# Kernel tuning notes

Measured on AMD Instinct MI355X. Metric: run time of the kernel, lower is better.

The kernel has to match this reference:

```python
import jax, jax.numpy as jnp
import numpy as np

N = 4194304          # flat pixel batch (~2 full 1080p frames)
NUM_CAMERAS = 8
NUM_FRAMES = 1000
EPS = 1e-6


def setup_inputs() -> dict:
    key = jax.random.key(0)
    ks = jax.random.split(key, 8)
    W, H = 1920, 1080
    exposure_params = 0.2 * jax.random.normal(ks[0], (NUM_FRAMES,), jnp.float32)
    vignetting_params = 0.05 * jax.random.normal(ks[1], (NUM_CAMERAS, 3, 5), jnp.float32)
    color_params = 0.05 * jax.random.normal(ks[2], (NUM_FRAMES, 8), jnp.float32)
    # CRF raw init matching the module: softplus-inverse of 1.0 with minima (0.3,0.3,0.1), offset 0
    def _sp_inv(x, m):
        return float(np.log(np.expm1(max(1e-5, x - m))))
    crf0 = jnp.array([_sp_inv(1.0, 0.3), _sp_inv(1.0, 0.3), _sp_inv(1.0, 0.1), 0.0], jnp.float32)
    crf_params = (jnp.broadcast_to(crf0, (NUM_CAMERAS, 3, 4))
                  + 0.05 * jax.random.normal(ks[3], (NUM_CAMERAS, 3, 4), jnp.float32))
    rgb = jax.random.uniform(ks[4], (N, 3), jnp.float32)
    pixel_coords = jax.random.uniform(ks[5], (N, 2), jnp.float32) * jnp.array([W, H], jnp.float32)
    camera_idcs = jax.random.randint(ks[6], (N,), 0, NUM_CAMERAS, jnp.int32)
    frame_idcs = jax.random.randint(ks[7], (N,), 0, NUM_FRAMES, jnp.int32)
    return dict(exposure_params=exposure_params, vignetting_params=vignetting_params,
                color_params=color_params, crf_params=crf_params, rgb=rgb,
                pixel_coords=pixel_coords, camera_idcs=camera_idcs, frame_idcs=frame_idcs,
                resolution_w=W, resolution_h=H)


def _ppisp(exposure_params, vignetting_params, color_params, crf_params,
           rgb, pixel_coords, camera_idcs, frame_idcs, resolution_w, resolution_h):
    # 1) per-frame exposure (EV scale)
    exp_scale = jnp.exp2(exposure_params[frame_idcs])[:, None]            # [N,1]
    x = rgb * exp_scale                                                    # [N,3]

    # 2) per-camera, per-channel radial vignetting: params = [cx, cy, a1, a2, a3]
    vig = vignetting_params[camera_idcs]                                   # [N,3,5]
    u = pixel_coords[:, 0] / jnp.float32(resolution_w) - 0.5               # [N]
    v = pixel_coords[:, 1] / jnp.float32(resolution_h) - 0.5               # [N]
    du = u[:, None] - vig[..., 0]                                          # [N,3]
    dv = v[:, None] - vig[..., 1]
    r2 = du * du + dv * dv                                                 # [N,3]
    falloff = 1.0 + r2 * (vig[..., 2] + r2 * (vig[..., 3] + r2 * vig[..., 4]))
    x = x * falloff

    # 3) per-frame color: WB gains (r,b) + off-diagonal 3x3 mixing matrix (8 params)
    cp = color_params[frame_idcs]                                          # [N,8]
    gains = jnp.stack([jnp.exp(cp[:, 0]), jnp.ones_like(cp[:, 0]), jnp.exp(cp[:, 1])], axis=-1)
    x = x * gains
    one = jnp.ones_like(cp[:, 0])
    M = jnp.stack([
        jnp.stack([one,      cp[:, 2], cp[:, 3]], axis=-1),
        jnp.stack([cp[:, 4], one,      cp[:, 5]], axis=-1),
        jnp.stack([cp[:, 6], cp[:, 7], one     ], axis=-1)], axis=-2)      # [N,3,3]
    x = jnp.einsum('nij,nj->ni', M, x)

    # 4) per-camera, per-channel 4-param sigmoid CRF, identity at init
    crf = crf_params[camera_idcs]                                          # [N,3,4]
    a = jax.nn.softplus(crf[..., 0]) + 0.3
    b = jax.nn.softplus(crf[..., 1]) + 0.3
    c = jax.nn.softplus(crf[..., 2]) + 0.1
    d = crf[..., 3]
    xc = jnp.clip(x, EPS, 1.0)
    xa = xc ** a
    out = xa / (xa + (c * (1.0 - xc) + EPS) ** b) + d                      # [N,3]
    return out


def reference(exposure_params, vignetting_params, color_params, crf_params,
              rgb, pixel_coords, camera_idcs, frame_idcs, resolution_w, resolution_h):
    return _ppisp(exposure_params, vignetting_params, color_params, crf_params,
                  rgb, pixel_coords, camera_idcs, frame_idcs, resolution_w, resolution_h)
```

## Files before the change

kernel.cpp:

```cpp
#include <hip/hip_runtime.h>


__device__ __forceinline__ unsigned bf16r(float x) {
    unsigned b = __float_as_uint(x);
    return (b + 0x7fffu + ((b >> 16) & 1u)) >> 16;
}
__device__ __forceinline__ unsigned packbf(float lo, float hi) {
    return bf16r(lo) | (bf16r(hi) << 16);
}
__device__ __forceinline__ float ulo(unsigned u) { return __uint_as_float(u << 16); }
__device__ __forceinline__ float uhi(unsigned u) { return __uint_as_float(u & 0xffff0000u); }

__global__ void ppisp_precompute(const float* __restrict__ expo,
                                 const float* __restrict__ colorp,
                                 const float* __restrict__ vigp,
                                 const float* __restrict__ crfp,
                                 unsigned* __restrict__ ftab,
                                 float* __restrict__ camtab,
                                 int num_frames, int ncam) {
    int tid = blockIdx.x * blockDim.x + threadIdx.x;
    if (tid < num_frames) {
        float e = exp2f(expo[tid]);
        const float* cp = colorp + tid * 8;
        float g_r = e * expf(cp[0]);
        float g_b = e * expf(cp[1]);
        unsigned* f = ftab + tid * 6;
        f[0] = packbf(g_r, e);
        f[1] = packbf(g_b, cp[2]);
        f[2] = packbf(cp[3], cp[4]);
        f[3] = packbf(cp[5], cp[6]);
        f[4] = packbf(cp[7], 0.f);
        f[5] = 0u;
    }
    if (tid < ncam * 3) {
        int c = tid / 3, ch = tid % 3;
        const float* vp = vigp + tid * 5;
        const float* cf = crfp + tid * 4;
        float* r = camtab + c * 28 + ch * 9;
        r[0] = vp[0];
        r[1] = vp[1];
        r[2] = vp[2];
        r[3] = vp[3];
        r[4] = vp[4];
        r[5] = log1pf(expf(cf[0])) + 0.3f;
        r[6] = log1pf(expf(cf[1])) + 0.3f;
        r[7] = log1pf(expf(cf[2])) + 0.1f;
        r[8] = cf[3];
        if (ch == 0) camtab[c * 28 + 27] = 0.f;
    }
}

__global__ __launch_bounds__(256, 5) void ppisp_main(
    const float4* __restrict__ rgb4,
    const float4* __restrict__ pc4,
    const int4*   __restrict__ cam4,
    const int4*   __restrict__ frm4,
    const uint2*  __restrict__ ftab2,
    const float4* __restrict__ camtab4,
    const int*    __restrict__ resw,
    const int*    __restrict__ resh,
    float4* __restrict__ out4,
    int ngroups, int groups_per_block, int num_frames, int ncam) {
    __shared__ uint2  sft[3000];
    __shared__ float4 scam[56];

    int tid = threadIdx.x;
    int nfw = num_frames * 3;
    for (int i = tid; i < nfw; i += 256) sft[i] = ftab2[i];
    if (tid < ncam * 7) scam[tid] = camtab4[tid];
    __syncthreads();

    float invW = 1.0f / (float)resw[0];
    float invH = 1.0f / (float)resh[0];

    int gbase = blockIdx.x * groups_per_block;
    int gend = gbase + groups_per_block;
    if (gend > ngroups) gend = ngroups;

    for (int g = gbase + tid; g < gend; g += 256) {
        float4 r0  = rgb4[(size_t)g * 3 + 0];
        float4 r1  = rgb4[(size_t)g * 3 + 1];
        float4 r2v = rgb4[(size_t)g * 3 + 2];
        float4 p0  = pc4[(size_t)g * 2 + 0];
        float4 p1  = pc4[(size_t)g * 2 + 1];
        int4 cams = cam4[g];
        int4 frms = frm4[g];

        float rgbp[4][3] = {{r0.x, r0.y, r0.z},
                            {r0.w, r1.x, r1.y},
                            {r1.z, r1.w, r2v.x},
                            {r2v.y, r2v.z, r2v.w}};
        float px[4] = {p0.x, p0.z, p1.x, p1.z};
        float py[4] = {p0.y, p0.w, p1.y, p1.z};
        py[2] = p1.y; py[3] = p1.w;
        py[0] = p0.y; py[1] = p0.w;
        int camA[4] = {cams.x, cams.y, cams.z, cams.w};
        int frmA[4] = {frms.x, frms.y, frms.z, frms.w};

        float o[12];

#pragma unroll
        for (int p = 0; p < 4; ++p) {
            int fb = frmA[p] * 3;
            uint2 A = sft[fb + 0];
            uint2 B = sft[fb + 1];
            unsigned Cw = sft[fb + 2].x;
            float g_r = ulo(A.x), g_g = uhi(A.x), g_b = ulo(A.y);
            float m01 = uhi(A.y), m02 = ulo(B.x), m10 = uhi(B.x);
            float m12 = ulo(B.y), m20 = uhi(B.y), m21 = ulo(Cw);

            int cb = camA[p] * 7;
            float4 q0 = scam[cb + 0];
            float4 q1 = scam[cb + 1];
            float4 q2 = scam[cb + 2];
            float4 q3 = scam[cb + 3];
            float4 q4 = scam[cb + 4];
            float4 q5 = scam[cb + 5];
            float4 q6 = scam[cb + 6];

            float u = px[p] * invW - 0.5f;
            float v = py[p] * invH - 0.5f;

            float cx0 = q0.x, cy0 = q0.y, a10 = q0.z, a20 = q0.w, a30 = q1.x;
            float aa0 = q1.y, bb0 = q1.z, cc0 = q1.w, dd0 = q2.x;
            float cx1 = q2.y, cy1 = q2.z, a11 = q2.w, a21 = q3.x, a31 = q3.y;
            float aa1 = q3.z, bb1 = q3.w, cc1 = q4.x, dd1 = q4.y;
            float cx2 = q4.z, cy2 = q4.w, a12 = q5.x, a22 = q5.y, a32 = q5.z;
            float aa2 = q5.w, bb2 = q6.x, cc2 = q6.y, dd2 = q6.z;

            float du0 = u - cx0, dv0 = v - cy0;
            float du1 = u - cx1, dv1 = v - cy1;
            float du2 = u - cx2, dv2 = v - cy2;
            float r20 = du0 * du0 + dv0 * dv0;
            float r21 = du1 * du1 + dv1 * dv1;
            float r22 = du2 * du2 + dv2 * dv2;
            float fa0 = 1.0f + r20 * (a10 + r20 * (a20 + r20 * a30));
            float fa1 = 1.0f + r21 * (a11 + r21 * (a21 + r21 * a31));
            float fa2 = 1.0f + r22 * (a12 + r22 * (a22 + r22 * a32));

            float x0 = rgbp[p][0] * g_r * fa0;
            float x1 = rgbp[p][1] * g_g * fa1;
            float x2 = rgbp[p][2] * g_b * fa2;

            float y0 = x0 + m01 * x1 + m02 * x2;
            float y1 = m10 * x0 + x1 + m12 * x2;
            float y2 = m20 * x0 + m21 * x1 + x2;

            float xc0 = fminf(fmaxf(y0, 1e-6f), 1.0f);
            float xc1 = fminf(fmaxf(y1, 1e-6f), 1.0f);
            float xc2 = fminf(fmaxf(y2, 1e-6f), 1.0f);

            float xa0 = __builtin_amdgcn_exp2f(aa0 * __builtin_amdgcn_logf(xc0));
            float xa1 = __builtin_amdgcn_exp2f(aa1 * __builtin_amdgcn_logf(xc1));
            float xa2 = __builtin_amdgcn_exp2f(aa2 * __builtin_amdgcn_logf(xc2));
            float t0 = cc0 * (1.0f - xc0) + 1e-6f;
            float t1 = cc1 * (1.0f - xc1) + 1e-6f;
            float t2 = cc2 * (1.0f - xc2) + 1e-6f;
            float tb0 = __builtin_amdgcn_exp2f(bb0 * __builtin_amdgcn_logf(t0));
            float tb1 = __builtin_amdgcn_exp2f(bb1 * __builtin_amdgcn_logf(t1));
            float tb2 = __builtin_amdgcn_exp2f(bb2 * __builtin_amdgcn_logf(t2));

            o[p * 3 + 0] = xa0 * __builtin_amdgcn_rcpf(xa0 + tb0) + dd0;
            o[p * 3 + 1] = xa1 * __builtin_amdgcn_rcpf(xa1 + tb1) + dd1;
            o[p * 3 + 2] = xa2 * __builtin_amdgcn_rcpf(xa2 + tb2) + dd2;
        }

        out4[(size_t)g * 3 + 0] = make_float4(o[0], o[1], o[2], o[3]);
        out4[(size_t)g * 3 + 1] = make_float4(o[4], o[5], o[6], o[7]);
        out4[(size_t)g * 3 + 2] = make_float4(o[8], o[9], o[10], o[11]);
    }
}

extern "C" void kernel_launch(void* const* d_in, const int* in_sizes, int n_in,
                              void* d_out, int out_size, void* d_ws, size_t ws_size,
                              hipStream_t stream) {
    const float* expo   = (const float*)d_in[0];
    const float* vigp   = (const float*)d_in[1];
    const float* colorp = (const float*)d_in[2];
    const float* crfp   = (const float*)d_in[3];
    const float* rgb    = (const float*)d_in[4];
    const float* pc     = (const float*)d_in[5];
    const int*   cam    = (const int*)d_in[6];
    const int*   frm    = (const int*)d_in[7];
    const int*   rw     = (const int*)d_in[8];
    const int*   rh     = (const int*)d_in[9];

    int num_frames = in_sizes[0];
    int ncam = in_sizes[1] / 15;
    int N = in_sizes[4] / 3;

    unsigned* ftab = (unsigned*)d_ws;
    size_t ftab_bytes = ((size_t)num_frames * 6 * sizeof(unsigned) + 255) & ~(size_t)255;
    float* camtab = (float*)((char*)d_ws + ftab_bytes);

    int pre_threads = 256;
    int pre_blocks = (num_frames + pre_threads - 1) / pre_threads;
    if (pre_blocks < 1) pre_blocks = 1;
    ppisp_precompute<<<pre_blocks, pre_threads, 0, stream>>>(
        expo, colorp, vigp, crfp, ftab, camtab, num_frames, ncam);

    int ngroups = N / 4;
    int blocks = 1536;
    int groups_per_block = (ngroups + blocks - 1) / blocks;
    ppisp_main<<<blocks, 256, 0, stream>>>(
        (const float4*)rgb, (const float4*)pc, (const int4*)cam, (const int4*)frm,
        (const uint2*)ftab, (const float4*)camtab, rw, rh, (float4*)d_out,
        ngroups, groups_per_block, num_frames, ncam);
}
```

Before: 182.6 us.

## Fuse table precompute into main kernel and use 1024-thread blocks

Removes the separate precompute launch. Each block now builds the per-frame bf16 table and the per-camera table directly in shared memory, so nothing round-trips through a global workspace. The frame table is repacked into one uint4 plus one float per frame, so each lookup is two LDS reads instead of three. Blocks grow to 1024 threads and the grid shrinks to 512 blocks, which spreads the redundant per-block precompute (exp per frame) over more pixels but cuts scheduling granularity.

```diff
diff --git a/kernel.cpp b/kernel.cpp
--- a/kernel.cpp
+++ b/kernel.cpp
@@ -11,32 +11,44 @@
 __device__ __forceinline__ float ulo(unsigned u) { return __uint_as_float(u << 16); }
 __device__ __forceinline__ float uhi(unsigned u) { return __uint_as_float(u & 0xffff0000u); }
 
-__global__ void ppisp_precompute(const float* __restrict__ expo,
-                                 const float* __restrict__ colorp,
-                                 const float* __restrict__ vigp,
-                                 const float* __restrict__ crfp,
-                                 unsigned* __restrict__ ftab,
-                                 float* __restrict__ camtab,
-                                 int num_frames, int ncam) {
-    int tid = blockIdx.x * blockDim.x + threadIdx.x;
-    if (tid < num_frames) {
-        float e = exp2f(expo[tid]);
-        const float* cp = colorp + tid * 8;
-        float g_r = e * expf(cp[0]);
-        float g_b = e * expf(cp[1]);
-        unsigned* f = ftab + tid * 6;
-        f[0] = packbf(g_r, e);
-        f[1] = packbf(g_b, cp[2]);
-        f[2] = packbf(cp[3], cp[4]);
-        f[3] = packbf(cp[5], cp[6]);
-        f[4] = packbf(cp[7], 0.f);
-        f[5] = 0u;
+__global__ __launch_bounds__(1024, 8) void ppisp_main(
+    const float*  __restrict__ expo,
+    const float*  __restrict__ vigp,
+    const float4* __restrict__ colorp4,
+    const float*  __restrict__ crfp,
+    const float4* __restrict__ rgb4,
+    const float4* __restrict__ pc4,
+    const int4*   __restrict__ cam4,
+    const int4*   __restrict__ frm4,
+    const int*    __restrict__ resw,
+    const int*    __restrict__ resh,
+    float4* __restrict__ out4,
+    int ngroups, int groups_per_block, int num_frames, int ncam)
+{
+    __shared__ uint4 sA[1000];
+    __shared__ float sB[1000];
+    __shared__ float scamf[224];
+
+    int tid = threadIdx.x;
+    for (int f = tid; f < num_frames; f += 1024) {
+        float e = exp2f(expo[f]);
+        float4 c0 = colorp4[f * 2 + 0];
+        float4 c1 = colorp4[f * 2 + 1];
+        float g_r = e * expf(c0.x);
+        float g_b = e * expf(c0.y);
+        uint4 A;
+        A.x = packbf(g_r, e);
+        A.y = packbf(g_b, c0.z);
+        A.z = packbf(c0.w, c1.x);
+        A.w = packbf(c1.y, c1.z);
+        sA[f] = A;
+        sB[f] = c1.w;
     }
     if (tid < ncam * 3) {
         int c = tid / 3, ch = tid % 3;
         const float* vp = vigp + tid * 5;
         const float* cf = crfp + tid * 4;
-        float* r = camtab + c * 28 + ch * 9;
+        float* r = scamf + c * 28 + ch * 9;
         r[0] = vp[0];
         r[1] = vp[1];
         r[2] = vp[2];
@@ -46,30 +58,11 @@
         r[6] = log1pf(expf(cf[1])) + 0.3f;
         r[7] = log1pf(expf(cf[2])) + 0.1f;
         r[8] = cf[3];
-        if (ch == 0) camtab[c * 28 + 27] = 0.f;
+        if (ch == 0) scamf[c * 28 + 27] = 0.f;
     }
-}
-
-__global__ __launch_bounds__(256, 5) void ppisp_main(
-    const float4* __restrict__ rgb4,
-    const float4* __restrict__ pc4,
-    const int4*   __restrict__ cam4,
-    const int4*   __restrict__ frm4,
-    const uint2*  __restrict__ ftab2,
-    const float4* __restrict__ camtab4,
-    const int*    __restrict__ resw,
-    const int*    __restrict__ resh,
-    float4* __restrict__ out4,
-    int ngroups, int groups_per_block, int num_frames, int ncam) {
-    __shared__ uint2  sft[3000];
-    __shared__ float4 scam[56];
-
-    int tid = threadIdx.x;
-    int nfw = num_frames * 3;
-    for (int i = tid; i < nfw; i += 256) sft[i] = ftab2[i];
-    if (tid < ncam * 7) scam[tid] = camtab4[tid];
     __syncthreads();
 
+    const float4* scam4 = (const float4*)scamf;
     float invW = 1.0f / (float)resw[0];
     float invH = 1.0f / (float)resh[0];
 
@@ -77,7 +70,7 @@
     int gend = gbase + groups_per_block;
     if (gend > ngroups) gend = ngroups;
 
-    for (int g = gbase + tid; g < gend; g += 256) {
+    for (int g = gbase + tid; g < gend; g += 1024) {
         float4 r0  = rgb4[(size_t)g * 3 + 0];
         float4 r1  = rgb4[(size_t)g * 3 + 1];
         float4 r2v = rgb4[(size_t)g * 3 + 2];
@@ -91,9 +84,7 @@
                             {r1.z, r1.w, r2v.x},
                             {r2v.y, r2v.z, r2v.w}};
         float px[4] = {p0.x, p0.z, p1.x, p1.z};
-        float py[4] = {p0.y, p0.w, p1.y, p1.z};
-        py[2] = p1.y; py[3] = p1.w;
-        py[0] = p0.y; py[1] = p0.w;
+        float py[4] = {p0.y, p0.w, p1.y, p1.w};
         int camA[4] = {cams.x, cams.y, cams.z, cams.w};
         int frmA[4] = {frms.x, frms.y, frms.z, frms.w};
 
@@ -101,22 +92,21 @@
 
 #pragma unroll
         for (int p = 0; p < 4; ++p) {
-            int fb = frmA[p] * 3;
-            uint2 A = sft[fb + 0];
-            uint2 B = sft[fb + 1];
-            unsigned Cw = sft[fb + 2].x;
-            float g_r = ulo(A.x), g_g = uhi(A.x), g_b = ulo(A.y);
-            float m01 = uhi(A.y), m02 = ulo(B.x), m10 = uhi(B.x);
-            float m12 = ulo(B.y), m20 = uhi(B.y), m21 = ulo(Cw);
+            uint4 A = sA[frmA[p]];
+            float m21 = sB[frmA[p]];
+            float g_r = ulo(A.x), g_g = uhi(A.x);
+            float g_b = ulo(A.y), m01 = uhi(A.y);
+            float m02 = ulo(A.z), m10 = uhi(A.z);
+            float m12 = ulo(A.w), m20 = uhi(A.w);
 
             int cb = camA[p] * 7;
-            float4 q0 = scam[cb + 0];
-            float4 q1 = scam[cb + 1];
-            float4 q2 = scam[cb + 2];
-            float4 q3 = scam[cb + 3];
-            float4 q4 = scam[cb + 4];
-            float4 q5 = scam[cb + 5];
-            float4 q6 = scam[cb + 6];
+            float4 q0 = scam4[cb + 0];
+            float4 q1 = scam4[cb + 1];
+            float4 q2 = scam4[cb + 2];
+            float4 q3 = scam4[cb + 3];
+            float4 q4 = scam4[cb + 4];
+            float4 q5 = scam4[cb + 5];
+            float4 q6 = scam4[cb + 6];
 
             float u = px[p] * invW - 0.5f;
             float v = py[p] * invH - 0.5f;
@@ -189,21 +179,12 @@
     int ncam = in_sizes[1] / 15;
     int N = in_sizes[4] / 3;
 
-    unsigned* ftab = (unsigned*)d_ws;
-    size_t ftab_bytes = ((size_t)num_frames * 6 * sizeof(unsigned) + 255) & ~(size_t)255;
-    float* camtab = (float*)((char*)d_ws + ftab_bytes);
-
-    int pre_threads = 256;
-    int pre_blocks = (num_frames + pre_threads - 1) / pre_threads;
-    if (pre_blocks < 1) pre_blocks = 1;
-    ppisp_precompute<<<pre_blocks, pre_threads, 0, stream>>>(
-        expo, colorp, vigp, crfp, ftab, camtab, num_frames, ncam);
-
     int ngroups = N / 4;
-    int blocks = 1536;
+    int blocks = 512;
     int groups_per_block = (ngroups + blocks - 1) / blocks;
-    ppisp_main<<<blocks, 256, 0, stream>>>(
+    ppisp_main<<<blocks, 1024, 0, stream>>>(
+        expo, vigp, (const float4*)colorp, crfp,
         (const float4*)rgb, (const float4*)pc, (const int4*)cam, (const int4*)frm,
-        (const uint2*)ftab, (const float4*)camtab, rw, rh, (float4*)d_out,
+        rw, rh, (float4*)d_out,
         ngroups, groups_per_block, num_frames, ncam);
 }
```

Result: slower. 220.6 us (+20.8%).
